# Kernel tuning notes

Measured on AMD Instinct MI355X. Metric: run time of the kernel, lower is better.

## Reference

```python
import jax, jax.numpy as jnp
import numpy as np
from jax import lax

B, T, D, NH = 8, 2048, 128, 4
HD = D // NH
EPS = 1e-5


def _ln(x, g, b):
    m = x.mean(-1, keepdims=True)
    v = ((x - m) ** 2).mean(-1, keepdims=True)
    return (x - m) / jnp.sqrt(v + EPS) * g + b


def _gelu(x):  # exact (erf) GELU, matching torch nn.GELU default
    return jax.nn.gelu(x, approximate=False)


def _forward(lob_feat, trade_feat, has_trade,
             ei_w, ei_b, ei_g, ei_beta, decay,
             in_proj_w, in_proj_b, out_proj_w, out_proj_b,
             cn_g, cn_b,
             lob_w, lob_b, lob_g, lob_beta,
             tr_w, tr_b, tr_g, tr_beta,
             of_w, of_b, of_g, of_beta):
    # event impact: Linear -> LayerNorm -> Tanh, gated by has_trade
    impact = jnp.tanh(_ln(trade_feat @ ei_w.T + ei_b, ei_g, ei_beta))
    impact = impact * has_trade[..., None]              # [B,T,D]

    # diagonal linear recurrence: state_t = sigmoid(decay) * state_{t-1} + impact_t
    d = jax.nn.sigmoid(decay)                           # [D]

    def step(s, x):
        s = d * s + x
        return s, s

    _, states = lax.scan(step, jnp.zeros_like(impact[:, 0]),
                         jnp.swapaxes(impact, 0, 1))    # [T,B,D]
    state_seq = jnp.swapaxes(states, 0, 1)              # [B,T,D]

    # fusion MLPs (dropout is identity in eval)
    lob_enh = _gelu(_ln(jnp.concatenate([lob_feat, state_seq], -1) @ lob_w.T + lob_b,
                        lob_g, lob_beta))
    trade_enh = _gelu(_ln(jnp.concatenate([trade_feat, state_seq], -1) @ tr_w.T + tr_b,
                          tr_g, tr_beta))

    # torch nn.MultiheadAttention (batch_first): q=lob_enh, k=v=trade_enh
    wq, wk, wv = in_proj_w[:D], in_proj_w[D:2 * D], in_proj_w[2 * D:]
    bq, bk, bv = in_proj_b[:D], in_proj_b[D:2 * D], in_proj_b[2 * D:]
    q = (lob_enh @ wq.T + bq).reshape(B, T, NH, HD)
    k = (trade_enh @ wk.T + bk).reshape(B, T, NH, HD)
    v = (trade_enh @ wv.T + bv).reshape(B, T, NH, HD)
    scores = jnp.einsum('bqhd,bkhd->bhqk', q, k) / jnp.sqrt(jnp.float32(HD))
    attn = jax.nn.softmax(scores, axis=-1)
    ctx = jnp.einsum('bhqk,bkhd->bqhd', attn, v).reshape(B, T, D)
    fused_attn = ctx @ out_proj_w.T + out_proj_b

    fused = _ln(lob_enh + fused_attn, cn_g, cn_b)
    output = _gelu(_ln(jnp.concatenate([fused, trade_enh], -1) @ of_w.T + of_b,
                       of_g, of_beta))
    return output


def setup_inputs() -> dict:
    key = jax.random.key(0)
    ks = jax.random.split(key, 20)
    s1 = 1.0 / np.sqrt(D)
    s2 = 1.0 / np.sqrt(2 * D)
    return {
        'lob_feat': jax.random.normal(ks[0], (B, T, D), jnp.float32),
        'trade_feat': jax.random.normal(ks[1], (B, T, D), jnp.float32),
        'has_trade': (jax.random.uniform(ks[2], (B, T)) < 0.5).astype(jnp.float32),
        'ei_w': jax.random.normal(ks[3], (D, D), jnp.float32) * s1,
        'ei_b': jnp.zeros((D,), jnp.float32),
        'ei_g': jnp.ones((D,), jnp.float32),
        'ei_beta': jnp.zeros((D,), jnp.float32),
        'decay': jnp.ones((D,), jnp.float32) * 0.9,
        'in_proj_w': jax.random.normal(ks[4], (3 * D, D), jnp.float32) * s1,
        'in_proj_b': jnp.zeros((3 * D,), jnp.float32),
        'out_proj_w': jax.random.normal(ks[5], (D, D), jnp.float32) * s1,
        'out_proj_b': jnp.zeros((D,), jnp.float32),
        'cn_g': jnp.ones((D,), jnp.float32),
        'cn_b': jnp.zeros((D,), jnp.float32),
        'lob_w': jax.random.normal(ks[6], (D, 2 * D), jnp.float32) * s2,
        'lob_b': jnp.zeros((D,), jnp.float32),
        'lob_g': jnp.ones((D,), jnp.float32),
        'lob_beta': jnp.zeros((D,), jnp.float32),
        'tr_w': jax.random.normal(ks[7], (D, 2 * D), jnp.float32) * s2,
        'tr_b': jnp.zeros((D,), jnp.float32),
        'tr_g': jnp.ones((D,), jnp.float32),
        'tr_beta': jnp.zeros((D,), jnp.float32),
        'of_w': jax.random.normal(ks[8], (D, 2 * D), jnp.float32) * s2,
        'of_b': jnp.zeros((D,), jnp.float32),
        'of_g': jnp.ones((D,), jnp.float32),
        'of_beta': jnp.zeros((D,), jnp.float32),
    }


def reference(lob_feat, trade_feat, has_trade,
              ei_w, ei_b, ei_g, ei_beta, decay,
              in_proj_w, in_proj_b, out_proj_w, out_proj_b,
              cn_g, cn_b,
              lob_w, lob_b, lob_g, lob_beta,
              tr_w, tr_b, tr_g, tr_beta,
              of_w, of_b, of_g, of_beta):
    return _forward(lob_feat, trade_feat, has_trade,
                    ei_w, ei_b, ei_g, ei_beta, decay,
                    in_proj_w, in_proj_b, out_proj_w, out_proj_b,
                    cn_g, cn_b,
                    lob_w, lob_b, lob_g, lob_beta,
                    tr_w, tr_b, tr_g, tr_beta,
                    of_w, of_b, of_g, of_beta)
```

## Files before the change

kernel.cpp:

```cpp
#include <hip/hip_runtime.h>
#include <math.h>


#define T_  2048

typedef short bf16x8 __attribute__((ext_vector_type(8)));
typedef float f32x4  __attribute__((ext_vector_type(4)));
typedef unsigned short ushort_t;

__device__ __forceinline__ float sigm(float x) { return 1.0f / (1.0f + __expf(-x)); }

__device__ __forceinline__ unsigned short f2bf(float x) {
    union { float f; unsigned u; } v; v.f = x;
    unsigned r = v.u + 0x7FFFu + ((v.u >> 16) & 1u);
    return (unsigned short)(r >> 16);
}
__device__ __forceinline__ float bf2f(ushort_t u) {
    union { unsigned u; float f; } v; v.u = ((unsigned)u) << 16; return v.f;
}

__device__ __forceinline__ float gelu_f(float x) {
    const float e = exp2f(fmaf(0.044715f * x, x * x, x) * -2.3022083f);
    return x * __builtin_amdgcn_rcpf(1.0f + e);
}
__device__ __forceinline__ float tanh_f(float y) {
    const float e = exp2f(y * 2.8853900818f);
    return 1.0f - 2.0f * __builtin_amdgcn_rcpf(e + 1.0f);
}

__global__ __launch_bounds__(256) void prep_kernel(
    const float* __restrict__ lob, const float* __restrict__ trade,
    const float* __restrict__ eiw, const float* __restrict__ ipw,
    const float* __restrict__ opw, const float* __restrict__ lobw,
    const float* __restrict__ trw, const float* __restrict__ ofw,
    ushort_t* __restrict__ pool)
{
    const size_t i8 = ((size_t)blockIdx.x * 256 + threadIdx.x) * 8;
    const float* src; size_t off;
    if      (i8 < 2097152) { src = lob;   off = 0; }
    else if (i8 < 4194304) { src = trade; off = 2097152; }
    else if (i8 < 4210688) { src = eiw;   off = 4194304; }
    else if (i8 < 4259840) { src = ipw;   off = 4210688; }
    else if (i8 < 4276224) { src = opw;   off = 4259840; }
    else if (i8 < 4308992) { src = lobw;  off = 4276224; }
    else if (i8 < 4341760) { src = trw;   off = 4308992; }
    else                   { src = ofw;   off = 4341760; }
    const float4 a = *(const float4*)(src + (i8 - off));
    const float4 b = *(const float4*)(src + (i8 - off) + 4);
    bf16x8 o;
    o[0] = (short)f2bf(a.x); o[1] = (short)f2bf(a.y);
    o[2] = (short)f2bf(a.z); o[3] = (short)f2bf(a.w);
    o[4] = (short)f2bf(b.x); o[5] = (short)f2bf(b.y);
    o[6] = (short)f2bf(b.z); o[7] = (short)f2bf(b.w);
    *(bf16x8*)(pool + i8) = o;
}

__global__ __launch_bounds__(256) void gemm_ei(
    const ushort_t* __restrict__ Xb0, const ushort_t* __restrict__ Wb,
    const float* __restrict__ bias, const float* __restrict__ gamma,
    const float* __restrict__ beta, const float* __restrict__ extra,
    ushort_t* __restrict__ outb)
{
    __shared__ float red[32][2][2];
    const int tid = threadIdx.x, wid = tid >> 6, lane = tid & 63;
    const int c2 = lane & 15, g = lane >> 4;
    const int rowblk = wid >> 1, chf = wid & 1, cb0 = chf * 4;
    const int R0 = blockIdx.x * 32 + rowblk * 16;

    f32x4 acc[4] = {};
#pragma unroll
    for (int ch = 0; ch < 4; ch++) {
        const bf16x8 a = *(const bf16x8*)(Xb0 + (size_t)(R0 + c2) * 128 + ch * 32 + g * 8);
#pragma unroll
        for (int j = 0; j < 4; j++) {
            const bf16x8 b = *(const bf16x8*)(Wb + (size_t)((cb0 + j) * 16 + c2) * 128 + ch * 32 + g * 8);
            acc[j] = __builtin_amdgcn_mfma_f32_16x16x32_bf16(a, b, acc[j], 0, 0, 0);
        }
    }
    float gm[4], bt[4];
#pragma unroll
    for (int j = 0; j < 4; j++) {
        const int col = (cb0 + j) * 16 + c2;
        const float bb = bias[col];
        gm[j] = gamma[col]; bt[j] = beta[col];
#pragma unroll
        for (int r = 0; r < 4; r++) acc[j][r] += bb;
    }
#pragma unroll
    for (int r = 0; r < 4; r++) {
        float s = 0.f, ss = 0.f;
#pragma unroll
        for (int j = 0; j < 4; j++) { const float v = acc[j][r]; s += v; ss = fmaf(v, v, ss); }
#pragma unroll
        for (int o = 8; o; o >>= 1) { s += __shfl_xor(s, o); ss += __shfl_xor(ss, o); }
        if (c2 == 0) {
            red[rowblk * 16 + 4 * g + r][chf][0] = s;
            red[rowblk * 16 + 4 * g + r][chf][1] = ss;
        }
    }
    __syncthreads();
#pragma unroll
    for (int r = 0; r < 4; r++) {
        const int lr = rowblk * 16 + 4 * g + r;
        const float S  = red[lr][0][0] + red[lr][1][0];
        const float SS = red[lr][0][1] + red[lr][1][1];
        const float mean = S * (1.0f / 128.0f);
        float var = SS * (1.0f / 128.0f) - mean * mean;
        var = fmaxf(var, 0.0f);
        const float rstd = rsqrtf(var + 1e-5f);
        const int R = blockIdx.x * 32 + lr;
        const float ext = extra[R];
#pragma unroll
        for (int j = 0; j < 4; j++) {
            const float y = (acc[j][r] - mean) * rstd * gm[j] + bt[j];
            outb[(size_t)R * 128 + (cb0 + j) * 16 + c2] = f2bf(tanh_f(y) * ext);
        }
    }
}

__global__ __launch_bounds__(256) void enh_qkv(
    const ushort_t* __restrict__ lobb, const ushort_t* __restrict__ trab,
    const ushort_t* __restrict__ stab,
    const ushort_t* __restrict__ lobw, const ushort_t* __restrict__ trw,
    const ushort_t* __restrict__ ipw, const float* __restrict__ ipb,
    const float* __restrict__ lob_b, const float* __restrict__ lob_g,
    const float* __restrict__ lob_beta,
    const float* __restrict__ tr_b, const float* __restrict__ tr_g,
    const float* __restrict__ tr_beta,
    float* __restrict__ lobe_f, ushort_t* __restrict__ tre_bf,
    ushort_t* __restrict__ qo, ushort_t* __restrict__ ko, ushort_t* __restrict__ vo)
{
    __shared__ ushort_t lob_t[32][136];
    __shared__ ushort_t tre_t[32][136];
    __shared__ ushort_t vls[128][36];
    __shared__ float red[32][2][4];
    const int tid = threadIdx.x, wid = tid >> 6, lane = tid & 63;
    const int c2 = lane & 15, g = lane >> 4;
    const int rowblk = wid >> 1, chf = wid & 1, cb0 = chf * 4;
    const int RB = blockIdx.x * 32;
    const int R0 = RB + rowblk * 16;

    f32x4 aL[4] = {}, aT[4] = {};
#pragma unroll
    for (int ch = 0; ch < 8; ch++) {
        const int kk = (ch & 3) * 32;
        bf16x8 xl, xt;
        if (ch < 4) {
            xl = *(const bf16x8*)(lobb + (size_t)(R0 + c2) * 128 + kk + g * 8);
            xt = *(const bf16x8*)(trab + (size_t)(R0 + c2) * 128 + kk + g * 8);
        } else {
            xl = *(const bf16x8*)(stab + (size_t)(R0 + c2) * 128 + kk + g * 8);
            xt = xl;
        }
#pragma unroll
        for (int j = 0; j < 4; j++) {
            const size_t wo = (size_t)((cb0 + j) * 16 + c2) * 256 + ch * 32 + g * 8;
            aL[j] = __builtin_amdgcn_mfma_f32_16x16x32_bf16(xl, *(const bf16x8*)(lobw + wo), aL[j], 0, 0, 0);
            aT[j] = __builtin_amdgcn_mfma_f32_16x16x32_bf16(xt, *(const bf16x8*)(trw + wo), aT[j], 0, 0, 0);
        }
    }
#pragma unroll
    for (int j = 0; j < 4; j++) {
        const int col = (cb0 + j) * 16 + c2;
        const float bL = lob_b[col], bT = tr_b[col];
#pragma unroll
        for (int r = 0; r < 4; r++) { aL[j][r] += bL; aT[j][r] += bT; }
    }
#pragma unroll
    for (int r = 0; r < 4; r++) {
        float sL = 0.f, ssL = 0.f, sT = 0.f, ssT = 0.f;
#pragma unroll
        for (int j = 0; j < 4; j++) {
            const float vL = aL[j][r], vT = aT[j][r];
            sL += vL; ssL = fmaf(vL, vL, ssL);
            sT += vT; ssT = fmaf(vT, vT, ssT);
        }
#pragma unroll
        for (int o = 8; o; o >>= 1) {
            sL += __shfl_xor(sL, o); ssL += __shfl_xor(ssL, o);
            sT += __shfl_xor(sT, o); ssT += __shfl_xor(ssT, o);
        }
        if (c2 == 0) {
            float* rd = red[rowblk * 16 + 4 * g + r][chf];
            rd[0] = sL; rd[1] = ssL; rd[2] = sT; rd[3] = ssT;
        }
    }
    __syncthreads();
#pragma unroll
    for (int r = 0; r < 4; r++) {
        const int lr = rowblk * 16 + 4 * g + r;
        const int R = RB + lr;
        const float SL  = red[lr][0][0] + red[lr][1][0];
        const float SSL = red[lr][0][1] + red[lr][1][1];
        const float ST  = red[lr][0][2] + red[lr][1][2];
        const float SST = red[lr][0][3] + red[lr][1][3];
        const float mL = SL * (1.0f / 128.0f), mT = ST * (1.0f / 128.0f);
        const float rL = rsqrtf(fmaxf(SSL * (1.0f / 128.0f) - mL * mL, 0.0f) + 1e-5f);
        const float rT = rsqrtf(fmaxf(SST * (1.0f / 128.0f) - mT * mT, 0.0f) + 1e-5f);
#pragma unroll
        for (int j = 0; j < 4; j++) {
            const int col = (cb0 + j) * 16 + c2;
            const float yL = gelu_f((aL[j][r] - mL) * rL * lob_g[col] + lob_beta[col]);
            const float yT = gelu_f((aT[j][r] - mT) * rT * tr_g[col] + tr_beta[col]);
            lobe_f[(size_t)R * 128 + col] = yL;
            lob_t[lr][col] = f2bf(yL);
            const ushort_t tb = f2bf(yT);
            tre_bf[(size_t)R * 128 + col] = tb;
            tre_t[lr][col] = tb;
        }
    }
    __syncthreads();

    const float qscale = 0.17677669529663687f * 1.4426950408889634f;
#pragma unroll
    for (int which = 0; which < 3; which++) {
        const ushort_t (*src)[136] = (which == 0) ? lob_t : tre_t;
        const ushort_t* Wp = ipw + (size_t)which * 16384;
        f32x4 pa[4] = {};
#pragma unroll
        for (int ch = 0; ch < 4; ch++) {
            const bf16x8 a = *(const bf16x8*)&src[rowblk * 16 + c2][ch * 32 + g * 8];
#pragma unroll
            for (int j = 0; j < 4; j++) {
                const bf16x8 b = *(const bf16x8*)(Wp + (size_t)((cb0 + j) * 16 + c2) * 128 + ch * 32 + g * 8);
                pa[j] = __builtin_amdgcn_mfma_f32_16x16x32_bf16(a, b, pa[j], 0, 0, 0);
            }
        }
        if (which < 2) {
            ushort_t* dst = (which == 0) ? qo : ko;
            const float sc = (which == 0) ? qscale : 1.0f;
#pragma unroll
            for (int j = 0; j < 4; j++) {
                const int col = (cb0 + j) * 16 + c2;
                const float bb = ipb[which * 128 + col];
                const int h = col >> 5, hd = col & 31;
#pragma unroll
                for (int r = 0; r < 4; r++) {
                    const int R = R0 + 4 * g + r;
                    const int b = R >> 11, t = R & 2047;
                    dst[(((size_t)b * 4 + h) * 2048 + t) * 32 + hd] = f2bf((pa[j][r] + bb) * sc);
                }
            }
        } else {
#pragma unroll
            for (int j = 0; j < 4; j++) {
                const int col = (cb0 + j) * 16 + c2;
                const float bb = ipb[256 + col];
#pragma unroll
                for (int r = 0; r < 4; r++)
                    vls[col][rowblk * 16 + 4 * g + r] = f2bf(pa[j][r] + bb);
            }
        }
    }
    __syncthreads();
    {
        const int col = tid >> 1, hf = tid & 1;
        const int h = col >> 5, hd = col & 31;
        const int b = RB >> 11;
        unsigned w[8];
#pragma unroll
        for (int e = 0; e < 8; e++) {
            const int p0 = hf * 16 + 2 * e;
            const int g2 = p0 >> 3, j2 = p0 & 7;
            const int lk = 4 * g2 + j2 + (j2 >= 4 ? 12 : 0);
            w[e] = (unsigned)vls[col][lk] | ((unsigned)vls[col][lk + 1] << 16);
        }
        ushort_t* dst = vo + (((size_t)b * 4 + h) * 32 + hd) * 2048 + (RB & 2047) + hf * 16;
        *(uint4*)dst       = *(const uint4*)&w[0];
        *(uint4*)(dst + 8) = *(const uint4*)&w[4];
    }
}

__global__ __launch_bounds__(256) void attn_kernel(
    const ushort_t* __restrict__ q, const ushort_t* __restrict__ k,
    const ushort_t* __restrict__ vtg,
    ushort_t* __restrict__ part, float* __restrict__ rs_part,
    float* __restrict__ m_part)
{
    __shared__ ushort_t ks[2][64][40];
    __shared__ ushort_t vt[2][32][72];
    const int tid = threadIdx.x, wid = tid >> 6, lane = tid & 63;
    const int c = lane & 15, g = lane >> 4;
    const int half = blockIdx.x & 1, qt = blockIdx.x >> 1;
    const int bh = blockIdx.y;
    const ushort_t* kb_ = k   + (size_t)bh * 65536 + (size_t)half * 1024 * 32;
    const ushort_t* vb_ = vtg + (size_t)bh * 65536 + (size_t)half * 1024;
    const int q0 = qt * 128 + wid * 32;

    const ushort_t* qbase = q + ((size_t)bh * 2048 + q0) * 32;
    const bf16x8 qf0 = *(const bf16x8*)(qbase + (size_t)c * 32 + g * 8);
    const bf16x8 qf1 = *(const bf16x8*)(qbase + (size_t)(16 + c) * 32 + g * 8);

    bf16x8 ones;
#pragma unroll
    for (int i = 0; i < 8; i++) ones[i] = (short)0x3F80;

    float m0 = 0.0f, m1 = 0.0f;
    f32x4 acc[2][2] = {};
    f32x4 racc[2] = {};

    const int srow = tid >> 2, ssg = tid & 3;
    const int vd = tid >> 3, vkg = tid & 7;

    {
        const bf16x8 kk8 = *(const bf16x8*)(kb_ + (size_t)srow * 32 + ssg * 8);
        const bf16x8 vv8 = *(const bf16x8*)(vb_ + (size_t)vd * 2048 + vkg * 8);
        *(bf16x8*)&ks[0][srow][ssg * 8] = kk8;
        *(bf16x8*)&vt[0][vd][vkg * 8] = vv8;
    }
    __syncthreads();

    for (int kt = 0; kt < 16; kt++) {
        const int cur = kt & 1;
        bf16x8 kk8, vv8;
        if (kt + 1 < 16) {
            kk8 = *(const bf16x8*)(kb_ + ((size_t)(kt + 1) * 64 + srow) * 32 + ssg * 8);
            vv8 = *(const bf16x8*)(vb_ + (size_t)vd * 2048 + (kt + 1) * 64 + vkg * 8);
        }

        f32x4 s0[4], s1[4];
        __builtin_amdgcn_s_setprio(1);
#pragma unroll
        for (int kb2 = 0; kb2 < 4; kb2++) {
            const bf16x8 kf = *(const bf16x8*)&ks[cur][kb2 * 16 + c][g * 8];
            f32x4 z = {};
            s0[kb2] = __builtin_amdgcn_mfma_f32_16x16x32_bf16(kf, qf0, z, 0, 0, 0);
            s1[kb2] = __builtin_amdgcn_mfma_f32_16x16x32_bf16(kf, qf1, z, 0, 0, 0);
        }
        __builtin_amdgcn_s_setprio(0);

        float lm = -1e30f;
#pragma unroll
        for (int kb2 = 0; kb2 < 4; kb2++) {
            lm = fmaxf(lm, fmaxf(fmaxf(s0[kb2][0], s0[kb2][1]), fmaxf(s0[kb2][2], s0[kb2][3])));
            lm = fmaxf(lm, fmaxf(fmaxf(s1[kb2][0], s1[kb2][1]), fmaxf(s1[kb2][2], s1[kb2][3])));
        }
        if (__any(lm > 80.0f || m0 != 0.0f || m1 != 0.0f)) {
            float l0 = -1e30f, l1 = -1e30f;
#pragma unroll
            for (int kb2 = 0; kb2 < 4; kb2++) {
#pragma unroll
                for (int r = 0; r < 4; r++) { l0 = fmaxf(l0, s0[kb2][r]); l1 = fmaxf(l1, s1[kb2][r]); }
            }
            l0 = fmaxf(l0, __shfl_xor(l0, 16)); l0 = fmaxf(l0, __shfl_xor(l0, 32));
            l1 = fmaxf(l1, __shfl_xor(l1, 16)); l1 = fmaxf(l1, __shfl_xor(l1, 32));
            const float n0 = fmaxf(m0, l0), n1 = fmaxf(m1, l1);
            const float a0 = exp2f(m0 - n0), a1 = exp2f(m1 - n1);
#pragma unroll
            for (int nb = 0; nb < 2; nb++)
#pragma unroll
                for (int r = 0; r < 4; r++) { acc[0][nb][r] *= a0; acc[1][nb][r] *= a1; }
#pragma unroll
            for (int r = 0; r < 4; r++) { racc[0][r] *= a0; racc[1][r] *= a1; }
            m0 = n0; m1 = n1;
#pragma unroll
            for (int kb2 = 0; kb2 < 4; kb2++)
#pragma unroll
                for (int r = 0; r < 4; r++) {
                    s0[kb2][r] = exp2f(s0[kb2][r] - m0);
                    s1[kb2][r] = exp2f(s1[kb2][r] - m1);
                }
        } else {
#pragma unroll
            for (int kb2 = 0; kb2 < 4; kb2++)
#pragma unroll
                for (int r = 0; r < 4; r++) {
                    s0[kb2][r] = exp2f(s0[kb2][r]);
                    s1[kb2][r] = exp2f(s1[kb2][r]);
                }
        }

        union { unsigned u[4]; bf16x8 v; } p0a, p0b, p1a, p1b;
        asm("v_cvt_pk_bf16_f32 %0, %1, %2" : "=v"(p0a.u[0]) : "v"(s0[0][0]), "v"(s0[0][1]));
        asm("v_cvt_pk_bf16_f32 %0, %1, %2" : "=v"(p0a.u[1]) : "v"(s0[0][2]), "v"(s0[0][3]));
        asm("v_cvt_pk_bf16_f32 %0, %1, %2" : "=v"(p0a.u[2]) : "v"(s0[1][0]), "v"(s0[1][1]));
        asm("v_cvt_pk_bf16_f32 %0, %1, %2" : "=v"(p0a.u[3]) : "v"(s0[1][2]), "v"(s0[1][3]));
        asm("v_cvt_pk_bf16_f32 %0, %1, %2" : "=v"(p0b.u[0]) : "v"(s0[2][0]), "v"(s0[2][1]));
        asm("v_cvt_pk_bf16_f32 %0, %1, %2" : "=v"(p0b.u[1]) : "v"(s0[2][2]), "v"(s0[2][3]));
        asm("v_cvt_pk_bf16_f32 %0, %1, %2" : "=v"(p0b.u[2]) : "v"(s0[3][0]), "v"(s0[3][1]));
        asm("v_cvt_pk_bf16_f32 %0, %1, %2" : "=v"(p0b.u[3]) : "v"(s0[3][2]), "v"(s0[3][3]));
        asm("v_cvt_pk_bf16_f32 %0, %1, %2" : "=v"(p1a.u[0]) : "v"(s1[0][0]), "v"(s1[0][1]));
        asm("v_cvt_pk_bf16_f32 %0, %1, %2" : "=v"(p1a.u[1]) : "v"(s1[0][2]), "v"(s1[0][3]));
        asm("v_cvt_pk_bf16_f32 %0, %1, %2" : "=v"(p1a.u[2]) : "v"(s1[1][0]), "v"(s1[1][1]));
        asm("v_cvt_pk_bf16_f32 %0, %1, %2" : "=v"(p1a.u[3]) : "v"(s1[1][2]), "v"(s1[1][3]));
        asm("v_cvt_pk_bf16_f32 %0, %1, %2" : "=v"(p1b.u[0]) : "v"(s1[2][0]), "v"(s1[2][1]));
        asm("v_cvt_pk_bf16_f32 %0, %1, %2" : "=v"(p1b.u[1]) : "v"(s1[2][2]), "v"(s1[2][3]));
        asm("v_cvt_pk_bf16_f32 %0, %1, %2" : "=v"(p1b.u[2]) : "v"(s1[3][0]), "v"(s1[3][1]));
        asm("v_cvt_pk_bf16_f32 %0, %1, %2" : "=v"(p1b.u[3]) : "v"(s1[3][2]), "v"(s1[3][3]));

        __builtin_amdgcn_s_setprio(1);
#pragma unroll
        for (int nb = 0; nb < 2; nb++) {
            const bf16x8 v0 = *(const bf16x8*)&vt[cur][nb * 16 + c][g * 8];
            const bf16x8 v1 = *(const bf16x8*)&vt[cur][nb * 16 + c][32 + g * 8];
            acc[0][nb] = __builtin_amdgcn_mfma_f32_16x16x32_bf16(v0, p0a.v, acc[0][nb], 0, 0, 0);
            acc[0][nb] = __builtin_amdgcn_mfma_f32_16x16x32_bf16(v1, p0b.v, acc[0][nb], 0, 0, 0);
            acc[1][nb] = __builtin_amdgcn_mfma_f32_16x16x32_bf16(v0, p1a.v, acc[1][nb], 0, 0, 0);
            acc[1][nb] = __builtin_amdgcn_mfma_f32_16x16x32_bf16(v1, p1b.v, acc[1][nb], 0, 0, 0);
        }
        racc[0] = __builtin_amdgcn_mfma_f32_16x16x32_bf16(ones, p0a.v, racc[0], 0, 0, 0);
        racc[0] = __builtin_amdgcn_mfma_f32_16x16x32_bf16(ones, p0b.v, racc[0], 0, 0, 0);
        racc[1] = __builtin_amdgcn_mfma_f32_16x16x32_bf16(ones, p1a.v, racc[1], 0, 0, 0);
        racc[1] = __builtin_amdgcn_mfma_f32_16x16x32_bf16(ones, p1b.v, racc[1], 0, 0, 0);
        __builtin_amdgcn_s_setprio(0);

        if (kt + 1 < 16) {
            *(bf16x8*)&ks[cur ^ 1][srow][ssg * 8] = kk8;
            *(bf16x8*)&vt[cur ^ 1][vd][vkg * 8] = vv8;
        }
        __syncthreads();
    }

    ushort_t* pb = part + (size_t)(half * 32 + bh) * 32 * 2048;
#pragma unroll
    for (int qf = 0; qf < 2; qf++) {
        const int qrow = q0 + qf * 16 + c;
#pragma unroll
        for (int nb = 0; nb < 2; nb++)
#pragma unroll
            for (int r = 0; r < 4; r++)
                pb[(size_t)(nb * 16 + 4 * g + r) * 2048 + qrow] = f2bf(acc[qf][nb][r]);
    }
    if (g == 0) {
        float* rsp = rs_part + (size_t)(half * 32 + bh) * 2048;
        float* mp  = m_part  + (size_t)(half * 32 + bh) * 2048;
        rsp[q0 + c]      = racc[0][0];
        rsp[q0 + 16 + c] = racc[1][0];
        mp[q0 + c]       = m0;
        mp[q0 + 16 + c]  = m1;
    }
}

__global__ __launch_bounds__(256) void attn_combine(
    const ushort_t* __restrict__ part, const float* __restrict__ rs_part,
    const float* __restrict__ m_part, ushort_t* __restrict__ ctx)
{
    const int bh = blockIdx.y, tb = blockIdx.x;
    const int b = bh >> 2, h = bh & 3;
    const int t = tb * 128 + (threadIdx.x >> 1);
    const int dh = threadIdx.x & 1;
    const float mA = m_part[(size_t)bh * 2048 + t];
    const float mB = m_part[(size_t)(32 + bh) * 2048 + t];
    const float rA = rs_part[(size_t)bh * 2048 + t];
    const float rB = rs_part[(size_t)(32 + bh) * 2048 + t];
    const float M = fmaxf(mA, mB);
    const float wA = exp2f(mA - M), wB = exp2f(mB - M);
    const float inv = __builtin_amdgcn_rcpf(fmaf(rA, wA, rB * wB));
    const ushort_t* pA = part + (size_t)bh * 32 * 2048;
    const ushort_t* pB = part + (size_t)(32 + bh) * 32 * 2048;
    ushort_t buf[16];
#pragma unroll
    for (int i = 0; i < 16; i++) {
        const int d = dh * 16 + i;
        const float v = fmaf(bf2f(pA[(size_t)d * 2048 + t]), wA,
                             bf2f(pB[(size_t)d * 2048 + t]) * wB) * inv;
        buf[i] = f2bf(v);
    }
    ushort_t* dst = ctx + ((size_t)(b * 2048 + t)) * 128 + h * 32 + dh * 16;
    *(uint4*)dst = *(const uint4*)&buf[0];
    *(uint4*)(dst + 8) = *(const uint4*)&buf[8];
}

__global__ __launch_bounds__(256) void out_fuse(
    const ushort_t* __restrict__ ctxb, const ushort_t* __restrict__ treb,
    const ushort_t* __restrict__ opw, const float* __restrict__ opb,
    const float* __restrict__ cn_g, const float* __restrict__ cn_b,
    const ushort_t* __restrict__ ofw, const float* __restrict__ of_b,
    const float* __restrict__ of_g, const float* __restrict__ of_beta,
    const float* __restrict__ lobe_f, float* __restrict__ out)
{
    __shared__ ushort_t fus_t[32][136];
    __shared__ float red[32][2][2];
    const int tid = threadIdx.x, wid = tid >> 6, lane = tid & 63;
    const int c2 = lane & 15, g = lane >> 4;
    const int rowblk = wid >> 1, chf = wid & 1, cb0 = chf * 4;
    const int RB = blockIdx.x * 32;
    const int R0 = RB + rowblk * 16;

    f32x4 acc[4] = {};
#pragma unroll
    for (int ch = 0; ch < 4; ch++) {
        const bf16x8 a = *(const bf16x8*)(ctxb + (size_t)(R0 + c2) * 128 + ch * 32 + g * 8);
#pragma unroll
        for (int j = 0; j < 4; j++) {
            const bf16x8 b = *(const bf16x8*)(opw + (size_t)((cb0 + j) * 16 + c2) * 128 + ch * 32 + g * 8);
            acc[j] = __builtin_amdgcn_mfma_f32_16x16x32_bf16(a, b, acc[j], 0, 0, 0);
        }
    }
#pragma unroll
    for (int j = 0; j < 4; j++) {
        const int col = (cb0 + j) * 16 + c2;
        const float bb = opb[col];
#pragma unroll
        for (int r = 0; r < 4; r++)
            acc[j][r] += bb + lobe_f[(size_t)(R0 + 4 * g + r) * 128 + col];
    }
#pragma unroll
    for (int r = 0; r < 4; r++) {
        float s = 0.f, ss = 0.f;
#pragma unroll
        for (int j = 0; j < 4; j++) { const float v = acc[j][r]; s += v; ss = fmaf(v, v, ss); }
#pragma unroll
        for (int o = 8; o; o >>= 1) { s += __shfl_xor(s, o); ss += __shfl_xor(ss, o); }
        if (c2 == 0) {
            red[rowblk * 16 + 4 * g + r][chf][0] = s;
            red[rowblk * 16 + 4 * g + r][chf][1] = ss;
        }
    }
    __syncthreads();
#pragma unroll
    for (int r = 0; r < 4; r++) {
        const int lr = rowblk * 16 + 4 * g + r;
        const float S  = red[lr][0][0] + red[lr][1][0];
        const float SS = red[lr][0][1] + red[lr][1][1];
        const float mean = S * (1.0f / 128.0f);
        const float rstd = rsqrtf(fmaxf(SS * (1.0f / 128.0f) - mean * mean, 0.0f) + 1e-5f);
#pragma unroll
        for (int j = 0; j < 4; j++) {
            const int col = (cb0 + j) * 16 + c2;
            fus_t[lr][col] = f2bf((acc[j][r] - mean) * rstd * cn_g[col] + cn_b[col]);
        }
    }
    __syncthreads();

    f32x4 a2[4] = {};
#pragma unroll
    for (int ch = 0; ch < 8; ch++) {
        bf16x8 a;
        if (ch < 4) a = *(const bf16x8*)&fus_t[rowblk * 16 + c2][ch * 32 + g * 8];
        else        a = *(const bf16x8*)(treb + (size_t)(R0 + c2) * 128 + (ch - 4) * 32 + g * 8);
#pragma unroll
        for (int j = 0; j < 4; j++) {
            const bf16x8 b = *(const bf16x8*)(ofw + (size_t)((cb0 + j) * 16 + c2) * 256 + ch * 32 + g * 8);
            a2[j] = __builtin_amdgcn_mfma_f32_16x16x32_bf16(a, b, a2[j], 0, 0, 0);
        }
    }
#pragma unroll
    for (int j = 0; j < 4; j++) {
        const float bb = of_b[(cb0 + j) * 16 + c2];
#pragma unroll
        for (int r = 0; r < 4; r++) a2[j][r] += bb;
    }
#pragma unroll
    for (int r = 0; r < 4; r++) {
        float s = 0.f, ss = 0.f;
#pragma unroll
        for (int j = 0; j < 4; j++) { const float v = a2[j][r]; s += v; ss = fmaf(v, v, ss); }
#pragma unroll
        for (int o = 8; o; o >>= 1) { s += __shfl_xor(s, o); ss += __shfl_xor(ss, o); }
        if (c2 == 0) {
            red[rowblk * 16 + 4 * g + r][chf][0] = s;
            red[rowblk * 16 + 4 * g + r][chf][1] = ss;
        }
    }
    __syncthreads();
#pragma unroll
    for (int r = 0; r < 4; r++) {
        const int lr = rowblk * 16 + 4 * g + r;
        const float S  = red[lr][0][0] + red[lr][1][0];
        const float SS = red[lr][0][1] + red[lr][1][1];
        const float mean = S * (1.0f / 128.0f);
        const float rstd = rsqrtf(fmaxf(SS * (1.0f / 128.0f) - mean * mean, 0.0f) + 1e-5f);
        const int R = RB + lr;
#pragma unroll
        for (int j = 0; j < 4; j++) {
            const int col = (cb0 + j) * 16 + c2;
            const float y = (a2[j][r] - mean) * rstd * of_g[col] + of_beta[col];
            out[(size_t)R * 128 + col] = gelu_f(y);
        }
    }
}

__global__ void scan_ends_kernel(const ushort_t* __restrict__ imp,
                                 const float* __restrict__ decay,
                                 float* __restrict__ ends)
{
    const int c = threadIdx.x;
    const int ch = blockIdx.x, b = blockIdx.y;
    const float d = sigm(decay[c]);
    const size_t base = ((size_t)b * T_ + ch * 64) * 128 + c;
    float s = 0.0f;
#pragma unroll 4
    for (int tl = 0; tl < 64; tl++)
        s = fmaf(d, s, bf2f(imp[base + (size_t)tl * 128]));
    ends[((size_t)b * 32 + ch) * 128 + c] = s;
}

__global__ void scan_carry_kernel(const float* __restrict__ ends,
                                  const float* __restrict__ decay,
                                  float* __restrict__ carry)
{
    const int c = threadIdx.x;
    const int b = blockIdx.x;
    const float d = sigm(decay[c]);
    float dl = d;
#pragma unroll
    for (int i = 0; i < 6; i++) dl *= dl;
    float e = 0.0f;
#pragma unroll
    for (int ch = 0; ch < 32; ch++) {
        carry[((size_t)b * 32 + ch) * 128 + c] = e;
        e = fmaf(dl, e, ends[((size_t)b * 32 + ch) * 128 + c]);
    }
}

__global__ void scan_fin_kernel(const ushort_t* __restrict__ imp,
                                const float* __restrict__ decay,
                                const float* __restrict__ carry,
                                ushort_t* __restrict__ stbf)
{
    const int c = threadIdx.x;
    const int ch = blockIdx.x, b = blockIdx.y;
    const float d = sigm(decay[c]);
    float s = carry[((size_t)b * 32 + ch) * 128 + c];
    const size_t base = ((size_t)b * T_ + ch * 64) * 128 + c;
#pragma unroll 4
    for (int tl = 0; tl < 64; tl++) {
        s = fmaf(d, s, bf2f(imp[base + (size_t)tl * 128]));
        stbf[base + (size_t)tl * 128] = f2bf(s);
    }
}

extern "C" void kernel_launch(void* const* d_in, const int* in_sizes, int n_in,
                              void* d_out, int out_size, void* d_ws, size_t ws_size,
                              hipStream_t stream)
{
    const float* lob_feat   = (const float*)d_in[0];
    const float* trade_feat = (const float*)d_in[1];
    const float* has_trade  = (const float*)d_in[2];
    const float* ei_w       = (const float*)d_in[3];
    const float* ei_b       = (const float*)d_in[4];
    const float* ei_g       = (const float*)d_in[5];
    const float* ei_beta    = (const float*)d_in[6];
    const float* decay      = (const float*)d_in[7];
    const float* in_proj_w  = (const float*)d_in[8];
    const float* in_proj_b  = (const float*)d_in[9];
    const float* out_proj_w = (const float*)d_in[10];
    const float* out_proj_b = (const float*)d_in[11];
    const float* cn_g       = (const float*)d_in[12];
    const float* cn_b       = (const float*)d_in[13];
    const float* lob_w      = (const float*)d_in[14];
    const float* lob_b      = (const float*)d_in[15];
    const float* lob_g      = (const float*)d_in[16];
    const float* lob_beta   = (const float*)d_in[17];
    const float* tr_w       = (const float*)d_in[18];
    const float* tr_b       = (const float*)d_in[19];
    const float* tr_g       = (const float*)d_in[20];
    const float* tr_beta    = (const float*)d_in[21];
    const float* of_w       = (const float*)d_in[22];
    const float* of_b       = (const float*)d_in[23];
    const float* of_g       = (const float*)d_in[24];
    const float* of_beta    = (const float*)d_in[25];

    char* W = (char*)d_ws;
    const size_t MB = 1u << 20;
    float*    lobe_f   = (float*)W;
    float*    carry    = (float*)(W + 8 * MB);
    float*    ends     = (float*)(W + 8 * MB + 256 * 1024);
    ushort_t* pool     = (ushort_t*)(W + 9 * MB);
    ushort_t* imp_bf   = (ushort_t*)(W + 18 * MB);
    ushort_t* state_bf = (ushort_t*)(W + 22 * MB);
    ushort_t* tre_bf   = (ushort_t*)(W + 26 * MB);
    ushort_t* q_bf     = (ushort_t*)(W + 30 * MB);
    ushort_t* k_bf     = (ushort_t*)(W + 34 * MB);
    ushort_t* vt_g     = (ushort_t*)(W + 38 * MB);
    ushort_t* ctx_bf   = (ushort_t*)(W + 42 * MB);
    ushort_t* part     = (ushort_t*)(W + 46 * MB);
    float*    rs_part  = (float*)(W + 54 * MB);
    float*    m_part   = (float*)(W + 54 * MB + 512 * 1024);

    ushort_t* lob_bf   = pool;
    ushort_t* trade_bf = pool + 2097152;
    ushort_t* eiw_bf   = pool + 4194304;
    ushort_t* ipw_bf   = pool + 4210688;
    ushort_t* opw_bf   = pool + 4259840;
    ushort_t* lobw_bf  = pool + 4276224;
    ushort_t* trw_bf   = pool + 4308992;
    ushort_t* ofw_bf   = pool + 4341760;

    const dim3 blk(256);

    prep_kernel<<<dim3(2136), blk, 0, stream>>>(lob_feat, trade_feat, ei_w, in_proj_w,
                                                out_proj_w, lob_w, tr_w, of_w, pool);
    gemm_ei<<<dim3(512), blk, 0, stream>>>(trade_bf, eiw_bf, ei_b, ei_g, ei_beta,
                                           has_trade, imp_bf);
    scan_ends_kernel<<<dim3(32, 8), dim3(128), 0, stream>>>(imp_bf, decay, ends);
    scan_carry_kernel<<<dim3(8), dim3(128), 0, stream>>>(ends, decay, carry);
    scan_fin_kernel<<<dim3(32, 8), dim3(128), 0, stream>>>(imp_bf, decay, carry, state_bf);
    enh_qkv<<<dim3(512), blk, 0, stream>>>(lob_bf, trade_bf, state_bf, lobw_bf, trw_bf,
                                           ipw_bf, in_proj_b, lob_b, lob_g, lob_beta,
                                           tr_b, tr_g, tr_beta, lobe_f, tre_bf,
                                           q_bf, k_bf, vt_g);
    attn_kernel<<<dim3(32, 32), blk, 0, stream>>>(q_bf, k_bf, vt_g, part, rs_part, m_part);
    attn_combine<<<dim3(16, 32), blk, 0, stream>>>(part, rs_part, m_part, ctx_bf);
    out_fuse<<<dim3(512), blk, 0, stream>>>(ctx_bf, tre_bf, opw_bf, out_proj_b, cn_g, cn_b,
                                            ofw_bf, of_b, of_g, of_beta, lobe_f, (float*)d_out);
}
```

Before: 144.2 us.

## Fuse split-KV attention combine into output projection and store lobe in bf16

Removes the separate attn_combine kernel. The attention kernel now writes its partial contexts in row-major [B,T,D] layout with packed bf16 conversion, and out_fuse merges the two halves using the softmax max and row-sum terms before the out-projection MFMA. The lob_enh residual is now stored in bf16 instead of fp32, which halves its traffic but adds rounding to the residual path. The softmax max reduction is also rewritten as a chain of three-input maxes.

```diff
diff --git a/kernel.cpp b/kernel.cpp
--- a/kernel.cpp
+++ b/kernel.cpp
@@ -27,6 +27,7 @@
     const float e = exp2f(y * 2.8853900818f);
     return 1.0f - 2.0f * __builtin_amdgcn_rcpf(e + 1.0f);
 }
+#define MX3(a, b, c) fmaxf(fmaxf((a), (b)), (c))
 
 __global__ __launch_bounds__(256) void prep_kernel(
     const float* __restrict__ lob, const float* __restrict__ trade,
@@ -127,7 +128,7 @@
     const float* __restrict__ lob_beta,
     const float* __restrict__ tr_b, const float* __restrict__ tr_g,
     const float* __restrict__ tr_beta,
-    float* __restrict__ lobe_f, ushort_t* __restrict__ tre_bf,
+    ushort_t* __restrict__ lobe_b, ushort_t* __restrict__ tre_bf,
     ushort_t* __restrict__ qo, ushort_t* __restrict__ ko, ushort_t* __restrict__ vo)
 {
     __shared__ ushort_t lob_t[32][136];
@@ -202,8 +203,9 @@
             const int col = (cb0 + j) * 16 + c2;
             const float yL = gelu_f((aL[j][r] - mL) * rL * lob_g[col] + lob_beta[col]);
             const float yT = gelu_f((aT[j][r] - mT) * rT * tr_g[col] + tr_beta[col]);
-            lobe_f[(size_t)R * 128 + col] = yL;
-            lob_t[lr][col] = f2bf(yL);
+            const ushort_t lb = f2bf(yL);
+            lobe_b[(size_t)R * 128 + col] = lb;
+            lob_t[lr][col] = lb;
             const ushort_t tb = f2bf(yT);
             tre_bf[(size_t)R * 128 + col] = tb;
             tre_t[lr][col] = tb;
@@ -282,7 +284,7 @@
     const int tid = threadIdx.x, wid = tid >> 6, lane = tid & 63;
     const int c = lane & 15, g = lane >> 4;
     const int half = blockIdx.x & 1, qt = blockIdx.x >> 1;
-    const int bh = blockIdx.y;
+    const int bh = blockIdx.y, b = bh >> 2, h = bh & 3;
     const ushort_t* kb_ = k   + (size_t)bh * 65536 + (size_t)half * 1024 * 32;
     const ushort_t* vb_ = vtg + (size_t)bh * 65536 + (size_t)half * 1024;
     const int q0 = qt * 128 + wid * 32;
@@ -329,12 +331,22 @@
         }
         __builtin_amdgcn_s_setprio(0);
 
-        float lm = -1e30f;
-#pragma unroll
-        for (int kb2 = 0; kb2 < 4; kb2++) {
-            lm = fmaxf(lm, fmaxf(fmaxf(s0[kb2][0], s0[kb2][1]), fmaxf(s0[kb2][2], s0[kb2][3])));
-            lm = fmaxf(lm, fmaxf(fmaxf(s1[kb2][0], s1[kb2][1]), fmaxf(s1[kb2][2], s1[kb2][3])));
-        }
+        float lm = MX3(s0[0][0], s0[0][1], s0[0][2]);
+        lm = MX3(lm, s0[0][3], s0[1][0]);
+        lm = MX3(lm, s0[1][1], s0[1][2]);
+        lm = MX3(lm, s0[1][3], s0[2][0]);
+        lm = MX3(lm, s0[2][1], s0[2][2]);
+        lm = MX3(lm, s0[2][3], s0[3][0]);
+        lm = MX3(lm, s0[3][1], s0[3][2]);
+        lm = MX3(lm, s0[3][3], s1[0][0]);
+        lm = MX3(lm, s1[0][1], s1[0][2]);
+        lm = MX3(lm, s1[0][3], s1[1][0]);
+        lm = MX3(lm, s1[1][1], s1[1][2]);
+        lm = MX3(lm, s1[1][3], s1[2][0]);
+        lm = MX3(lm, s1[2][1], s1[2][2]);
+        lm = MX3(lm, s1[2][3], s1[3][0]);
+        lm = MX3(lm, s1[3][1], s1[3][2]);
+        lm = fmaxf(lm, s1[3][3]);
         if (__any(lm > 80.0f || m0 != 0.0f || m1 != 0.0f)) {
             float l0 = -1e30f, l1 = -1e30f;
 #pragma unroll
@@ -411,15 +423,19 @@
         __syncthreads();
     }
 
-    ushort_t* pb = part + (size_t)(half * 32 + bh) * 32 * 2048;
+    ushort_t* pb = part + (size_t)half * 2097152;
 #pragma unroll
     for (int qf = 0; qf < 2; qf++) {
         const int qrow = q0 + qf * 16 + c;
-#pragma unroll
-        for (int nb = 0; nb < 2; nb++)
-#pragma unroll
-            for (int r = 0; r < 4; r++)
-                pb[(size_t)(nb * 16 + 4 * g + r) * 2048 + qrow] = f2bf(acc[qf][nb][r]);
+        ushort_t* dst = pb + ((size_t)(b * 2048 + qrow)) * 128 + h * 32;
+#pragma unroll
+        for (int nb = 0; nb < 2; nb++) {
+            unsigned w0, w1;
+            asm("v_cvt_pk_bf16_f32 %0, %1, %2" : "=v"(w0) : "v"(acc[qf][nb][0]), "v"(acc[qf][nb][1]));
+            asm("v_cvt_pk_bf16_f32 %0, %1, %2" : "=v"(w1) : "v"(acc[qf][nb][2]), "v"(acc[qf][nb][3]));
+            uint2 wv; wv.x = w0; wv.y = w1;
+            *(uint2*)(dst + nb * 16 + 4 * g) = wv;
+        }
     }
     if (g == 0) {
         float* rsp = rs_part + (size_t)(half * 32 + bh) * 2048;
@@ -431,43 +447,15 @@
     }
 }
 
-__global__ __launch_bounds__(256) void attn_combine(
-    const ushort_t* __restrict__ part, const float* __restrict__ rs_part,
-    const float* __restrict__ m_part, ushort_t* __restrict__ ctx)
-{
-    const int bh = blockIdx.y, tb = blockIdx.x;
-    const int b = bh >> 2, h = bh & 3;
-    const int t = tb * 128 + (threadIdx.x >> 1);
-    const int dh = threadIdx.x & 1;
-    const float mA = m_part[(size_t)bh * 2048 + t];
-    const float mB = m_part[(size_t)(32 + bh) * 2048 + t];
-    const float rA = rs_part[(size_t)bh * 2048 + t];
-    const float rB = rs_part[(size_t)(32 + bh) * 2048 + t];
-    const float M = fmaxf(mA, mB);
-    const float wA = exp2f(mA - M), wB = exp2f(mB - M);
-    const float inv = __builtin_amdgcn_rcpf(fmaf(rA, wA, rB * wB));
-    const ushort_t* pA = part + (size_t)bh * 32 * 2048;
-    const ushort_t* pB = part + (size_t)(32 + bh) * 32 * 2048;
-    ushort_t buf[16];
-#pragma unroll
-    for (int i = 0; i < 16; i++) {
-        const int d = dh * 16 + i;
-        const float v = fmaf(bf2f(pA[(size_t)d * 2048 + t]), wA,
-                             bf2f(pB[(size_t)d * 2048 + t]) * wB) * inv;
-        buf[i] = f2bf(v);
-    }
-    ushort_t* dst = ctx + ((size_t)(b * 2048 + t)) * 128 + h * 32 + dh * 16;
-    *(uint4*)dst = *(const uint4*)&buf[0];
-    *(uint4*)(dst + 8) = *(const uint4*)&buf[8];
-}
-
 __global__ __launch_bounds__(256) void out_fuse(
-    const ushort_t* __restrict__ ctxb, const ushort_t* __restrict__ treb,
+    const ushort_t* __restrict__ ctxA, const ushort_t* __restrict__ ctxB,
+    const float* __restrict__ rs_part, const float* __restrict__ m_part,
+    const ushort_t* __restrict__ treb,
     const ushort_t* __restrict__ opw, const float* __restrict__ opb,
     const float* __restrict__ cn_g, const float* __restrict__ cn_b,
     const ushort_t* __restrict__ ofw, const float* __restrict__ of_b,
     const float* __restrict__ of_g, const float* __restrict__ of_beta,
-    const float* __restrict__ lobe_f, float* __restrict__ out)
+    const ushort_t* __restrict__ lobe_b, float* __restrict__ out)
 {
     __shared__ ushort_t fus_t[32][136];
     __shared__ float red[32][2][2];
@@ -477,14 +465,38 @@
     const int RB = blockIdx.x * 32;
     const int R0 = RB + rowblk * 16;
 
+    const int rowA = R0 + c2;
+    const int bb2 = rowA >> 11, tt = rowA & 2047;
+    float fA[4], fB[4];
+#pragma unroll
+    for (int h = 0; h < 4; h++) {
+        const int bh = bb2 * 4 + h;
+        const float mA = m_part[(size_t)bh * 2048 + tt];
+        const float mB = m_part[(size_t)(32 + bh) * 2048 + tt];
+        const float rA = rs_part[(size_t)bh * 2048 + tt];
+        const float rB = rs_part[(size_t)(32 + bh) * 2048 + tt];
+        const float M = fmaxf(mA, mB);
+        const float wA = exp2f(mA - M), wB = exp2f(mB - M);
+        const float inv = __builtin_amdgcn_rcpf(fmaf(rA, wA, rB * wB));
+        fA[h] = wA * inv; fB[h] = wB * inv;
+    }
+
     f32x4 acc[4] = {};
 #pragma unroll
     for (int ch = 0; ch < 4; ch++) {
-        const bf16x8 a = *(const bf16x8*)(ctxb + (size_t)(R0 + c2) * 128 + ch * 32 + g * 8);
+        const bf16x8 aA = *(const bf16x8*)(ctxA + (size_t)rowA * 128 + ch * 32 + g * 8);
+        const bf16x8 aB = *(const bf16x8*)(ctxB + (size_t)rowA * 128 + ch * 32 + g * 8);
+        union { unsigned u[4]; bf16x8 v; } am;
+#pragma unroll
+        for (int i = 0; i < 4; i++) {
+            const float e0 = bf2f((ushort_t)aA[2 * i]) * fA[ch] + bf2f((ushort_t)aB[2 * i]) * fB[ch];
+            const float e1 = bf2f((ushort_t)aA[2 * i + 1]) * fA[ch] + bf2f((ushort_t)aB[2 * i + 1]) * fB[ch];
+            asm("v_cvt_pk_bf16_f32 %0, %1, %2" : "=v"(am.u[i]) : "v"(e0), "v"(e1));
+        }
 #pragma unroll
         for (int j = 0; j < 4; j++) {
             const bf16x8 b = *(const bf16x8*)(opw + (size_t)((cb0 + j) * 16 + c2) * 128 + ch * 32 + g * 8);
-            acc[j] = __builtin_amdgcn_mfma_f32_16x16x32_bf16(a, b, acc[j], 0, 0, 0);
+            acc[j] = __builtin_amdgcn_mfma_f32_16x16x32_bf16(am.v, b, acc[j], 0, 0, 0);
         }
     }
 #pragma unroll
@@ -493,7 +505,7 @@
         const float bb = opb[col];
 #pragma unroll
         for (int r = 0; r < 4; r++)
-            acc[j][r] += bb + lobe_f[(size_t)(R0 + 4 * g + r) * 128 + col];
+            acc[j][r] += bb + bf2f(lobe_b[(size_t)(R0 + 4 * g + r) * 128 + col]);
     }
 #pragma unroll
     for (int r = 0; r < 4; r++) {
@@ -654,7 +666,7 @@
 
     char* W = (char*)d_ws;
     const size_t MB = 1u << 20;
-    float*    lobe_f   = (float*)W;
+    ushort_t* lobe_b   = (ushort_t*)W;
     float*    carry    = (float*)(W + 8 * MB);
     float*    ends     = (float*)(W + 8 * MB + 256 * 1024);
     ushort_t* pool     = (ushort_t*)(W + 9 * MB);
@@ -664,10 +676,9 @@
     ushort_t* q_bf     = (ushort_t*)(W + 30 * MB);
     ushort_t* k_bf     = (ushort_t*)(W + 34 * MB);
     ushort_t* vt_g     = (ushort_t*)(W + 38 * MB);
-    ushort_t* ctx_bf   = (ushort_t*)(W + 42 * MB);
-    ushort_t* part     = (ushort_t*)(W + 46 * MB);
-    float*    rs_part  = (float*)(W + 54 * MB);
-    float*    m_part   = (float*)(W + 54 * MB + 512 * 1024);
+    ushort_t* part     = (ushort_t*)(W + 42 * MB);
+    float*    rs_part  = (float*)(W + 50 * MB);
+    float*    m_part   = (float*)(W + 50 * MB + 512 * 1024);
 
     ushort_t* lob_bf   = pool;
     ushort_t* trade_bf = pool + 2097152;
@@ -677,6 +688,9 @@
     ushort_t* lobw_bf  = pool + 4276224;
     ushort_t* trw_bf   = pool + 4308992;
     ushort_t* ofw_bf   = pool + 4341760;
+
+    ushort_t* ctxA = part;
+    ushort_t* ctxB = part + 2097152;
 
     const dim3 blk(256);
 
@@ -689,10 +703,10 @@
     scan_fin_kernel<<<dim3(32, 8), dim3(128), 0, stream>>>(imp_bf, decay, carry, state_bf);
     enh_qkv<<<dim3(512), blk, 0, stream>>>(lob_bf, trade_bf, state_bf, lobw_bf, trw_bf,
                                            ipw_bf, in_proj_b, lob_b, lob_g, lob_beta,
-                                           tr_b, tr_g, tr_beta, lobe_f, tre_bf,
+                                           tr_b, tr_g, tr_beta, lobe_b, tre_bf,
                                            q_bf, k_bf, vt_g);
     attn_kernel<<<dim3(32, 32), blk, 0, stream>>>(q_bf, k_bf, vt_g, part, rs_part, m_part);
-    attn_combine<<<dim3(16, 32), blk, 0, stream>>>(part, rs_part, m_part, ctx_bf);
-    out_fuse<<<dim3(512), blk, 0, stream>>>(ctx_bf, tre_bf, opw_bf, out_proj_b, cn_g, cn_b,
-                                            ofw_bf, of_b, of_g, of_beta, lobe_f, (float*)d_out);
-}
+    out_fuse<<<dim3(512), blk, 0, stream>>>(ctxA, ctxB, rs_part, m_part, tre_bf,
+                                            opw_bf, out_proj_b, cn_g, cn_b,
+                                            ofw_bf, of_b, of_g, of_beta, lobe_b, (float*)d_out);
+}
```

New measurement: 139.7 us (median of 2 runs). 1.03x faster.
